# Kernel optimization log

Hardware: AMD Instinct MI355X
Metric: run time of the kernel (lower is better)

## Reference

```python
import jax, jax.numpy as jnp
import numpy as np

N, C_IN, C_OUT, T, V = 64, 64, 64, 300, 25
INTER_C = C_OUT // 4
NUM_SUBSET = 3
BN_EPS = 1e-5


def setup_inputs() -> dict:
    key = jax.random.key(0)
    ks = jax.random.split(key, 12)
    w_scale = 0.05  # keep attention logits in a sane range
    return {
        "x": jax.random.normal(ks[0], (N, C_IN, T, V), jnp.float32),
        "A": jax.random.uniform(ks[1], (NUM_SUBSET, V, V), jnp.float32),
        "graph_attn": jnp.ones((NUM_SUBSET, V, V), jnp.float32),
        "g_w": jax.random.normal(ks[2], (NUM_SUBSET, C_OUT, C_IN), jnp.float32) * w_scale,
        "g_b": jax.random.normal(ks[3], (NUM_SUBSET, C_OUT), jnp.float32) * w_scale,
        "a_w": jax.random.normal(ks[4], (NUM_SUBSET, INTER_C, C_IN), jnp.float32) * w_scale,
        "a_b": jax.random.normal(ks[5], (NUM_SUBSET, INTER_C), jnp.float32) * w_scale,
        "b_w": jax.random.normal(ks[6], (NUM_SUBSET, INTER_C, C_IN), jnp.float32) * w_scale,
        "b_b": jax.random.normal(ks[7], (NUM_SUBSET, INTER_C), jnp.float32) * w_scale,
        "bn_gamma": jax.random.uniform(ks[8], (C_OUT,), jnp.float32, 0.5, 1.5),
        "bn_beta": jax.random.normal(ks[9], (C_OUT,), jnp.float32) * 0.1,
        "bn_mean": jax.random.normal(ks[10], (C_OUT,), jnp.float32) * 0.1,
        "bn_var": jax.random.uniform(ks[11], (C_OUT,), jnp.float32, 0.5, 1.5),
    }


def _conv1x1(x, w, b):
    # 1x1 Conv2d over channel dim of [N, C, T, V]
    return jnp.einsum('nctv,oc->notv', x, w) + b[None, :, None, None]


def reference(x, A, graph_attn, g_w, g_b, a_w, a_b, b_w, b_b,
              bn_gamma, bn_beta, bn_mean, bn_var):
    A_full = A + graph_attn  # [3, V, V]
    hidden = None
    for i in range(NUM_SUBSET):
        A1 = _conv1x1(x, a_w[i], a_b[i]).transpose(0, 3, 1, 2)  # [N, V, inter_c, T]
        A2 = _conv1x1(x, b_w[i], b_b[i])                        # [N, inter_c, T, V]
        # [N, V, W, T] attention logits, softmax over axis -2 (W)
        S = jnp.einsum('nvct,nctw->nvwt', A1, A2) / INTER_C
        S = jax.nn.softmax(S, axis=-2)
        S = S + A_full[i][None, :, :, None]
        # faithful to torch: sum S over its first spatial axis, elementwise on x
        z = _conv1x1(jnp.einsum('nctv,nwvt->nctv', x, S), g_w[i], g_b[i])
        hidden = z if hidden is None else hidden + z
    # inference-mode BatchNorm2d
    inv = jax.lax.rsqrt(bn_var + BN_EPS)
    h = (hidden - bn_mean[None, :, None, None]) * (bn_gamma * inv)[None, :, None, None] \
        + bn_beta[None, :, None, None]
    # in_channels == out_channels -> identity residual
    h = h + x
    return jax.nn.relu(h)
```

## Files before the change

### kernel.cpp

```cpp
#include <hip/hip_runtime.h>
#include <math.h>


typedef __attribute__((ext_vector_type(8)))  short bf8;
typedef __attribute__((ext_vector_type(4)))  short bf4;
typedef __attribute__((ext_vector_type(4)))  float f4;
typedef __attribute__((ext_vector_type(16))) float f16v;

#define TT    5
#define COLS  125
#define COLSP 128
#define XROW  72
#define PQROW 40

__device__ __forceinline__ short f2bf(float f) {
  union { float f; unsigned u; } v; v.f = f;
  unsigned u = v.u;
  u += 0x7fffu + ((u >> 16) & 1u);
  return (short)(u >> 16);
}
__device__ __forceinline__ float bf2f(short s) {
  union { unsigned u; float f; } v;
  v.u = ((unsigned)(unsigned short)s) << 16;
  return v.f;
}
__device__ __forceinline__ float rsum16(float v) {
  v += __shfl_xor(v, 1);
  v += __shfl_xor(v, 2);
  v += __shfl_xor(v, 4);
  v += __shfl_xor(v, 8);
  return v;
}

__launch_bounds__(256, 5)
__global__ void tagc_v4_kernel(
    const float* __restrict__ x,
    const float* __restrict__ A,
    const float* __restrict__ G,
    const float* __restrict__ g_w,
    const float* __restrict__ g_b,
    const float* __restrict__ a_w,
    const float* __restrict__ a_b,
    const float* __restrict__ b_w,
    const float* __restrict__ b_b,
    const float* __restrict__ bn_g,
    const float* __restrict__ bn_b,
    const float* __restrict__ bn_m,
    const float* __restrict__ bn_v,
    float* __restrict__ out)
{
  __shared__ __align__(16) short Xb[COLSP * XROW];
  __shared__ __align__(16) short PQt[COLSP * PQROW];
  __shared__ float sv[TT * 28];
  __shared__ float colA[75];

  const int tid  = threadIdx.x;
  const int wave = tid >> 6;
  const int lane = tid & 63;
  const int l15  = lane & 15;
  const int quad = lane >> 4;
  const int l31  = lane & 31;
  const int hl   = lane >> 5;
  const int n    = blockIdx.y;
  const int t0   = blockIdx.x * TT;

  if (tid < 75) {
    int i = tid / 25, v = tid - 25 * i;
    float s = 0.f;
    for (int a = 0; a < 25; ++a)
      s += A[i * 625 + a * 25 + v] + G[i * 625 + a * 25 + v];
    colA[i * 25 + v] = s;
  }

  {
    const float* xb = x + (long)n * 480000 + t0 * 25;
    #pragma unroll
    for (int k = 0; k < 8; ++k) {
      int idx = k * 256 + tid;
      int c4  = idx >> 7;
      int col = idx & 127;
      bool ok = (col < COLS);
      bf4 wv;
      #pragma unroll
      for (int j = 0; j < 4; ++j) {
        float g = ok ? xb[(4 * c4 + j) * 7500 + col] : 0.f;
        wv[j] = f2bf(g);
      }
      *(bf4*)&Xb[col * XROW + 4 * c4] = wv;
    }
  }

  f16v R0, R1;
  #pragma unroll
  for (int r = 0; r < 16; ++r) { R0[r] = 0.f; R1[r] = 0.f; }

  __syncthreads();

  for (int i = 0; i < 3; ++i) {
    {
      const int mt  = wave & 1;
      const int ntb = (wave >> 1) * 4;
      const float* W  = (mt ? b_w : a_w) + i * 1024;
      const float* Bv = (mt ? b_b : a_b) + i * 16;

      bf8 Af[2];
      #pragma unroll
      for (int kk = 0; kk < 2; ++kk) {
        const float* p = W + l15 * 64 + kk * 32 + quad * 8;
        f4 u0 = *(const f4*)p;
        f4 u1 = *(const f4*)(p + 4);
        bf8 a;
        a[0]=f2bf(u0[0]); a[1]=f2bf(u0[1]); a[2]=f2bf(u0[2]); a[3]=f2bf(u0[3]);
        a[4]=f2bf(u1[0]); a[5]=f2bf(u1[1]); a[6]=f2bf(u1[2]); a[7]=f2bf(u1[3]);
        Af[kk] = a;
      }
      float bias[4];
      #pragma unroll
      for (int r = 0; r < 4; ++r) bias[r] = Bv[quad * 4 + r];

      #pragma unroll
      for (int j = 0; j < 4; ++j) {
        int nt = ntb + j;
        bf8 B0 = *(const bf8*)&Xb[(nt * 16 + l15) * XROW + quad * 8];
        bf8 B1 = *(const bf8*)&Xb[(nt * 16 + l15) * XROW + 32 + quad * 8];
        f4 acc = {0.f, 0.f, 0.f, 0.f};
        acc = __builtin_amdgcn_mfma_f32_16x16x32_bf16(Af[0], B0, acc, 0, 0, 0);
        acc = __builtin_amdgcn_mfma_f32_16x16x32_bf16(Af[1], B1, acc, 0, 0, 0);
        int col = nt * 16 + l15;
        bf4 w;
        #pragma unroll
        for (int r = 0; r < 4; ++r) w[r] = f2bf(acc[r] + bias[r]);
        *(bf4*)&PQt[col * PQROW + mt * 16 + quad * 4] = w;
      }
    }
    __syncthreads();

    for (int tsel = wave; tsel < TT; tsel += 4) {
      f4 sacc[2][2];
      #pragma unroll
      for (int am = 0; am < 2; ++am) {
        bf8 Afr = {0,0,0,0,0,0,0,0};
        if (quad < 2 && (am * 16 + l15) < 25)
          Afr = *(const bf8*)&PQt[(tsel * 25 + am * 16 + l15) * PQROW + quad * 8];
        #pragma unroll
        for (int wm = 0; wm < 2; ++wm) {
          bf8 Bfr = {0,0,0,0,0,0,0,0};
          if (quad < 2 && (wm * 16 + l15) < 25)
            Bfr = *(const bf8*)&PQt[(tsel * 25 + wm * 16 + l15) * PQROW + 16 + quad * 8];
          f4 z = {0.f, 0.f, 0.f, 0.f};
          sacc[am][wm] = __builtin_amdgcn_mfma_f32_16x16x32_bf16(Afr, Bfr, z, 0, 0, 0);
        }
      }
      const bool w1ok = (l15 < 9);
      float cs0 = 0.f, cs1 = 0.f;
      #pragma unroll
      for (int am = 0; am < 2; ++am) {
        #pragma unroll
        for (int r = 0; r < 4; ++r) {
          float e0 = __expf(sacc[am][0][r] * 0.0625f);
          float e1 = w1ok ? __expf(sacc[am][1][r] * 0.0625f) : 0.f;
          float d  = rsum16(e0 + e1);
          float rd = 1.f / d;
          int a = am * 16 + quad * 4 + r;
          if (a < 25) { cs0 += e0 * rd; cs1 += e1 * rd; }
        }
      }
      cs0 += __shfl_xor(cs0, 16); cs0 += __shfl_xor(cs0, 32);
      cs1 += __shfl_xor(cs1, 16); cs1 += __shfl_xor(cs1, 32);
      if (quad == 0) {
        sv[tsel * 28 + l15] = cs0 + colA[i * 25 + l15];
        if (l15 < 9)
          sv[tsel * 28 + 16 + l15] = cs1 + colA[i * 25 + 16 + l15];
      }
    }
    __syncthreads();

    {
      const int trow = wave >> 1;
      const int tcb  = wave & 1;
      bf8 Ag[4];
      #pragma unroll
      for (int kk = 0; kk < 4; ++kk) {
        const float* p = g_w + i * 4096 + (trow * 32 + l31) * 64 + kk * 16 + hl * 8;
        f4 u0 = *(const f4*)p;
        f4 u1 = *(const f4*)(p + 4);
        bf8 a;
        a[0]=f2bf(u0[0]); a[1]=f2bf(u0[1]); a[2]=f2bf(u0[2]); a[3]=f2bf(u0[3]);
        a[4]=f2bf(u1[0]); a[5]=f2bf(u1[1]); a[6]=f2bf(u1[2]); a[7]=f2bf(u1[3]);
        Ag[kk] = a;
      }
      #pragma unroll
      for (int tix = 0; tix < 2; ++tix) {
        int colb = (tcb + tix * 2) * 32;
        f16v za;
        #pragma unroll
        for (int r = 0; r < 16; ++r) za[r] = 0.f;
        #pragma unroll
        for (int kk = 0; kk < 4; ++kk) {
          bf8 Bf = *(const bf8*)&Xb[(colb + l31) * XROW + kk * 16 + hl * 8];
          za = __builtin_amdgcn_mfma_f32_32x32x16_bf16(Ag[kk], Bf, za, 0, 0, 0);
        }
        int col  = colb + l31;
        int colc = col < COLS ? col : (COLS - 1);
        int t = colc / 25, v = colc - 25 * t;
        float sval = sv[t * 28 + v];
        if (tix == 0) {
          #pragma unroll
          for (int r = 0; r < 16; ++r) R0[r] += za[r] * sval;
        } else {
          #pragma unroll
          for (int r = 0; r < 16; ++r) R1[r] += za[r] * sval;
        }
      }
    }
  }

  {
    const int trow = wave >> 1;
    const int tcb  = wave & 1;
    float* obase = out + (long)n * 480000 + t0 * 25;
    #pragma unroll
    for (int rg = 0; rg < 4; ++rg) {
      int ob = trow * 32 + rg * 8 + hl * 4;
      f4 bg = *(const f4*)(bn_g + ob);
      f4 bb = *(const f4*)(bn_b + ob);
      f4 bm = *(const f4*)(bn_m + ob);
      f4 bv = *(const f4*)(bn_v + ob);
      f4 g0 = *(const f4*)(g_b + ob);
      f4 g1 = *(const f4*)(g_b + 64 + ob);
      f4 g2 = *(const f4*)(g_b + 128 + ob);
      float scl[4], shf[4], gbs[4];
      #pragma unroll
      for (int r = 0; r < 4; ++r) {
        float sc = bg[r] * rsqrtf(bv[r] + 1e-5f);
        scl[r] = sc;
        shf[r] = bb[r] - bm[r] * sc;
        gbs[r] = g0[r] + g1[r] + g2[r];
      }
      #pragma unroll
      for (int tix = 0; tix < 2; ++tix) {
        int col = (tcb + tix * 2) * 32 + l31;
        if (col < COLS) {
          bf4 res = *(const bf4*)&Xb[col * XROW + ob];
          #pragma unroll
          for (int r = 0; r < 4; ++r) {
            float acc = tix ? R1[rg * 4 + r] : R0[rg * 4 + r];
            float h = (acc + gbs[r]) * scl[r] + shf[r] + bf2f(res[r]);
            obase[(long)(ob + r) * 7500 + col] = fmaxf(h, 0.f);
          }
        }
      }
    }
  }
}

extern "C" void kernel_launch(void* const* d_in, const int* in_sizes, int n_in,
                              void* d_out, int out_size, void* d_ws, size_t ws_size,
                              hipStream_t stream) {
  (void)in_sizes; (void)n_in; (void)d_ws; (void)ws_size; (void)out_size;
  dim3 grid(300 / TT, 64);
  tagc_v4_kernel<<<grid, dim3(256), 0, stream>>>(
      (const float*)d_in[0],  (const float*)d_in[1],  (const float*)d_in[2],
      (const float*)d_in[3],  (const float*)d_in[4],  (const float*)d_in[5],
      (const float*)d_in[6],  (const float*)d_in[7],  (const float*)d_in[8],
      (const float*)d_in[9],  (const float*)d_in[10], (const float*)d_in[11],
      (const float*)d_in[12], (float*)d_out);
}
```

Baseline: 364.6 us.

## Precompute bf16 weights and BN constants in a prep kernel, remap block order

Adds a small prep kernel that converts the attention and output conv weights to bf16, precomputes the column sums of A+graph_attn, and folds the BN scale/shift plus summed conv biases into two per-channel vectors, all stored in the workspace. The main kernel now loads bf16 weights directly and skips the per-block weight conversion, column-sum computation and BN constant computation. The block index is also remapped so that neighbouring blocks take different batch samples, which changes the order in which x is read. The cost is an extra kernel launch and a dependency on workspace buffers.

```diff
diff --git a/kernel.cpp b/kernel.cpp
--- a/kernel.cpp
+++ b/kernel.cpp
@@ -1,4 +1,5 @@
 #include <hip/hip_runtime.h>
+#include <hip/hip_bf16.h>
 #include <math.h>
 
 
@@ -13,11 +14,17 @@
 #define XROW  72
 #define PQROW 40
 
+#define WS_AW    0
+#define WS_BW    6144
+#define WS_GW    12288
+#define WS_COLA  36864
+#define WS_SCL   37376
+#define WS_SHF   37632
+#define WS_END   37888
+
 __device__ __forceinline__ short f2bf(float f) {
-  union { float f; unsigned u; } v; v.f = f;
-  unsigned u = v.u;
-  u += 0x7fffu + ((u >> 16) & 1u);
-  return (short)(u >> 16);
+  __hip_bfloat16 h = __float2bfloat16(f);
+  return __builtin_bit_cast(short, h);
 }
 __device__ __forceinline__ float bf2f(short s) {
   union { unsigned u; float f; } v;
@@ -32,21 +39,73 @@
   return v;
 }
 
+__global__ void tagc_prep(
+    const float* __restrict__ A,    const float* __restrict__ G,
+    const float* __restrict__ g_w,  const float* __restrict__ g_b,
+    const float* __restrict__ a_w,  const float* __restrict__ b_w,
+    const float* __restrict__ bn_g, const float* __restrict__ bn_b,
+    const float* __restrict__ bn_m, const float* __restrict__ bn_v,
+    short* __restrict__ aw_bf, short* __restrict__ bw_bf,
+    short* __restrict__ gw_bf, float* __restrict__ colA3,
+    float* __restrict__ scl,   float* __restrict__ shf2)
+{
+  const int b = blockIdx.x, tid = threadIdx.x;
+  if (b < 12) {
+    int base = b * 1024 + tid * 4;
+    f4 v = *(const f4*)(g_w + base);
+    bf4 o;
+    #pragma unroll
+    for (int r = 0; r < 4; ++r) o[r] = f2bf(v[r]);
+    *(bf4*)(gw_bf + base) = o;
+  } else if (b == 12) {
+    #pragma unroll
+    for (int g = 0; g < 3; ++g) {
+      int base = g * 1024 + tid * 4;
+      f4 v = *(const f4*)(a_w + base);
+      bf4 o;
+      #pragma unroll
+      for (int r = 0; r < 4; ++r) o[r] = f2bf(v[r]);
+      *(bf4*)(aw_bf + base) = o;
+    }
+  } else if (b == 13) {
+    #pragma unroll
+    for (int g = 0; g < 3; ++g) {
+      int base = g * 1024 + tid * 4;
+      f4 v = *(const f4*)(b_w + base);
+      bf4 o;
+      #pragma unroll
+      for (int r = 0; r < 4; ++r) o[r] = f2bf(v[r]);
+      *(bf4*)(bw_bf + base) = o;
+    }
+  } else if (b == 14) {
+    if (tid < 75) {
+      int i = tid / 25, v = tid - 25 * i;
+      float s = 0.f;
+      for (int a = 0; a < 25; ++a)
+        s += A[i * 625 + a * 25 + v] + G[i * 625 + a * 25 + v];
+      colA3[tid] = s;
+    }
+  } else {
+    if (tid < 64) {
+      float sc  = bn_g[tid] * rsqrtf(bn_v[tid] + 1e-5f);
+      float gbs = g_b[tid] + g_b[64 + tid] + g_b[128 + tid];
+      scl[tid]  = sc;
+      shf2[tid] = bn_b[tid] - bn_m[tid] * sc + gbs * sc;
+    }
+  }
+}
+
 __launch_bounds__(256, 5)
-__global__ void tagc_v4_kernel(
+__global__ void tagc_v5_kernel(
     const float* __restrict__ x,
-    const float* __restrict__ A,
-    const float* __restrict__ G,
-    const float* __restrict__ g_w,
-    const float* __restrict__ g_b,
-    const float* __restrict__ a_w,
     const float* __restrict__ a_b,
-    const float* __restrict__ b_w,
     const float* __restrict__ b_b,
-    const float* __restrict__ bn_g,
-    const float* __restrict__ bn_b,
-    const float* __restrict__ bn_m,
-    const float* __restrict__ bn_v,
+    const short* __restrict__ aw_bf,
+    const short* __restrict__ bw_bf,
+    const short* __restrict__ gw_bf,
+    const float* __restrict__ colA3,
+    const float* __restrict__ sclp,
+    const float* __restrict__ shf2p,
     float* __restrict__ out)
 {
   __shared__ __align__(16) short Xb[COLSP * XROW];
@@ -61,24 +120,21 @@
   const int quad = lane >> 4;
   const int l31  = lane & 31;
   const int hl   = lane >> 5;
-  const int n    = blockIdx.y;
-  const int t0   = blockIdx.x * TT;
-
-  if (tid < 75) {
-    int i = tid / 25, v = tid - 25 * i;
-    float s = 0.f;
-    for (int a = 0; a < 25; ++a)
-      s += A[i * 625 + a * 25 + v] + G[i * 625 + a * 25 + v];
-    colA[i * 25 + v] = s;
-  }
+
+  const int lin = blockIdx.y * 60 + blockIdx.x;
+  const int idx = lin >> 3;
+  const int n   = ((lin & 7) << 3) + idx / 60;
+  const int t0  = (idx % 60) * TT;
+
+  if (tid < 75) colA[tid] = colA3[tid];
 
   {
     const float* xb = x + (long)n * 480000 + t0 * 25;
     #pragma unroll
     for (int k = 0; k < 8; ++k) {
-      int idx = k * 256 + tid;
-      int c4  = idx >> 7;
-      int col = idx & 127;
+      int idxs = k * 256 + tid;
+      int c4  = idxs >> 7;
+      int col = idxs & 127;
       bool ok = (col < COLS);
       bf4 wv;
       #pragma unroll
@@ -100,20 +156,13 @@
     {
       const int mt  = wave & 1;
       const int ntb = (wave >> 1) * 4;
-      const float* W  = (mt ? b_w : a_w) + i * 1024;
+      const short* Wb = (mt ? bw_bf : aw_bf) + i * 1024;
       const float* Bv = (mt ? b_b : a_b) + i * 16;
 
       bf8 Af[2];
-      #pragma unroll
-      for (int kk = 0; kk < 2; ++kk) {
-        const float* p = W + l15 * 64 + kk * 32 + quad * 8;
-        f4 u0 = *(const f4*)p;
-        f4 u1 = *(const f4*)(p + 4);
-        bf8 a;
-        a[0]=f2bf(u0[0]); a[1]=f2bf(u0[1]); a[2]=f2bf(u0[2]); a[3]=f2bf(u0[3]);
-        a[4]=f2bf(u1[0]); a[5]=f2bf(u1[1]); a[6]=f2bf(u1[2]); a[7]=f2bf(u1[3]);
-        Af[kk] = a;
-      }
+      Af[0] = *(const bf8*)(Wb + l15 * 64 + quad * 8);
+      Af[1] = *(const bf8*)(Wb + l15 * 64 + 32 + quad * 8);
+
       float bias[4];
       #pragma unroll
       for (int r = 0; r < 4; ++r) bias[r] = Bv[quad * 4 + r];
@@ -178,17 +227,12 @@
     {
       const int trow = wave >> 1;
       const int tcb  = wave & 1;
+      const short* gp = gw_bf + i * 4096 + (trow * 32 + l31) * 64;
       bf8 Ag[4];
       #pragma unroll
-      for (int kk = 0; kk < 4; ++kk) {
-        const float* p = g_w + i * 4096 + (trow * 32 + l31) * 64 + kk * 16 + hl * 8;
-        f4 u0 = *(const f4*)p;
-        f4 u1 = *(const f4*)(p + 4);
-        bf8 a;
-        a[0]=f2bf(u0[0]); a[1]=f2bf(u0[1]); a[2]=f2bf(u0[2]); a[3]=f2bf(u0[3]);
-        a[4]=f2bf(u1[0]); a[5]=f2bf(u1[1]); a[6]=f2bf(u1[2]); a[7]=f2bf(u1[3]);
-        Ag[kk] = a;
-      }
+      for (int kk = 0; kk < 4; ++kk)
+        Ag[kk] = *(const bf8*)(gp + kk * 16 + hl * 8);
+
       #pragma unroll
       for (int tix = 0; tix < 2; ++tix) {
         int colb = (tcb + tix * 2) * 32;
@@ -222,21 +266,8 @@
     #pragma unroll
     for (int rg = 0; rg < 4; ++rg) {
       int ob = trow * 32 + rg * 8 + hl * 4;
-      f4 bg = *(const f4*)(bn_g + ob);
-      f4 bb = *(const f4*)(bn_b + ob);
-      f4 bm = *(const f4*)(bn_m + ob);
-      f4 bv = *(const f4*)(bn_v + ob);
-      f4 g0 = *(const f4*)(g_b + ob);
-      f4 g1 = *(const f4*)(g_b + 64 + ob);
-      f4 g2 = *(const f4*)(g_b + 128 + ob);
-      float scl[4], shf[4], gbs[4];
-      #pragma unroll
-      for (int r = 0; r < 4; ++r) {
-        float sc = bg[r] * rsqrtf(bv[r] + 1e-5f);
-        scl[r] = sc;
-        shf[r] = bb[r] - bm[r] * sc;
-        gbs[r] = g0[r] + g1[r] + g2[r];
-      }
+      f4 sc = *(const f4*)(sclp + ob);
+      f4 sh = *(const f4*)(shf2p + ob);
       #pragma unroll
       for (int tix = 0; tix < 2; ++tix) {
         int col = (tcb + tix * 2) * 32 + l31;
@@ -245,7 +276,7 @@
           #pragma unroll
           for (int r = 0; r < 4; ++r) {
             float acc = tix ? R1[rg * 4 + r] : R0[rg * 4 + r];
-            float h = (acc + gbs[r]) * scl[r] + shf[r] + bf2f(res[r]);
+            float h = acc * sc[r] + sh[r] + bf2f(res[r]);
             obase[(long)(ob + r) * 7500 + col] = fmaxf(h, 0.f);
           }
         }
@@ -257,12 +288,27 @@
 extern "C" void kernel_launch(void* const* d_in, const int* in_sizes, int n_in,
                               void* d_out, int out_size, void* d_ws, size_t ws_size,
                               hipStream_t stream) {
-  (void)in_sizes; (void)n_in; (void)d_ws; (void)ws_size; (void)out_size;
+  (void)in_sizes; (void)n_in; (void)ws_size; (void)out_size;
+  char* ws = (char*)d_ws;
+  short* aw_bf = (short*)(ws + WS_AW);
+  short* bw_bf = (short*)(ws + WS_BW);
+  short* gw_bf = (short*)(ws + WS_GW);
+  float* colA3 = (float*)(ws + WS_COLA);
+  float* scl   = (float*)(ws + WS_SCL);
+  float* shf2  = (float*)(ws + WS_SHF);
+
+  tagc_prep<<<dim3(16), dim3(256), 0, stream>>>(
+      (const float*)d_in[1],  (const float*)d_in[2],
+      (const float*)d_in[3],  (const float*)d_in[4],
+      (const float*)d_in[5],  (const float*)d_in[7],
+      (const float*)d_in[9],  (const float*)d_in[10],
+      (const float*)d_in[11], (const float*)d_in[12],
+      aw_bf, bw_bf, gw_bf, colA3, scl, shf2);
+
   dim3 grid(300 / TT, 64);
-  tagc_v4_kernel<<<grid, dim3(256), 0, stream>>>(
-      (const float*)d_in[0],  (const float*)d_in[1],  (const float*)d_in[2],
-      (const float*)d_in[3],  (const float*)d_in[4],  (const float*)d_in[5],
-      (const float*)d_in[6],  (const float*)d_in[7],  (const float*)d_in[8],
-      (const float*)d_in[9],  (const float*)d_in[10], (const float*)d_in[11],
-      (const float*)d_in[12], (float*)d_out);
-}
+  tagc_v5_kernel<<<grid, dim3(256), 0, stream>>>(
+      (const float*)d_in[0],
+      (const float*)d_in[6],  (const float*)d_in[8],
+      aw_bf, bw_bf, gw_bf, colA3, scl, shf2,
+      (float*)d_out);
+}
```

Result: faster. 329.5 us (-9.6%).
